# Optimization experiments

Measured on AMD Instinct MI355X. Metric: run time of the kernel, lower is better.

Reference implementation:

```python
import jax, jax.numpy as jnp
import numpy as np

S, B, D, H, E, HID = 512, 16, 768, 12, 8, 3072
HD = D // H
EPS = 1e-5


def _ln(x, w, b):
    m = jnp.mean(x, axis=-1, keepdims=True)
    v = jnp.var(x, axis=-1, keepdims=True)
    return (x - m) * jax.lax.rsqrt(v + EPS) * w + b


def setup_inputs() -> dict:
    key = jax.random.key(0)
    ks = jax.random.split(key, 9)
    n = lambda k, *sh: jax.random.normal(k, sh, dtype=jnp.float32) * 0.02
    return dict(
        x=jax.random.normal(ks[0], (S, B, D), dtype=jnp.float32),
        ln1_w=jnp.ones((D,), jnp.float32), ln1_b=jnp.zeros((D,), jnp.float32),
        wq=n(ks[1], D, D), bq=jnp.zeros((D,), jnp.float32),
        wk=n(ks[2], D, D), bk=jnp.zeros((D,), jnp.float32),
        wv=n(ks[3], D, D), bv=jnp.zeros((D,), jnp.float32),
        wo=n(ks[4], D, D), bo=jnp.zeros((D,), jnp.float32),
        ln2_w=jnp.ones((D,), jnp.float32), ln2_b=jnp.zeros((D,), jnp.float32),
        wg=n(ks[5], D, E), bg=jnp.zeros((E,), jnp.float32),
        w1=n(ks[6], E, D, HID), b1=jnp.zeros((E, HID), jnp.float32),
        w2=n(ks[7], E, HID, D), b2=jnp.zeros((E, D), jnp.float32),
    )


def _block(x, ln1_w, ln1_b, wq, bq, wk, bk, wv, bv, wo, bo,
           ln2_w, ln2_b, wg, bg, w1, b1, w2, b2):
    # --- attention: source uses query = norm1(x), key = value = x ---
    q_in = _ln(x, ln1_w, ln1_b)
    q = (q_in @ wq + bq).reshape(S, B, H, HD)
    k = (x @ wk + bk).reshape(S, B, H, HD)
    v = (x @ wv + bv).reshape(S, B, H, HD)
    scores = jnp.einsum('sbhd,tbhd->bhst', q, k) * (1.0 / HD ** 0.5)
    p = jax.nn.softmax(scores, axis=-1)
    attn = jnp.einsum('bhst,tbhd->sbhd', p, v).reshape(S, B, D)
    x = x + attn @ wo + bo
    # --- top-1 MoE MLP on norm2(x) ---
    t = _ln(x, ln2_w, ln2_b).reshape(S * B, D)   # [T, D] routed tokens
    logits = t @ wg + bg                          # [T, E]
    probs = jax.nn.softmax(logits, axis=-1)
    idx = jnp.argmax(logits, axis=-1)             # top-1 expert per token
    gate = jnp.take_along_axis(probs, idx[:, None], axis=-1)   # [T, 1]
    comb = jax.nn.one_hot(idx, E, dtype=t.dtype) * gate        # [T, E]

    def expert(w1e, b1e, w2e, b2e):
        return jax.nn.gelu(t @ w1e + b1e, approximate=False) @ w2e + b2e

    y = jax.vmap(expert)(w1, b1, w2, b2)          # [E, T, D]
    moe = jnp.einsum('te,etd->td', comb, y).reshape(S, B, D)
    return x + moe


def reference(x, ln1_w, ln1_b, wq, bq, wk, bk, wv, bv, wo, bo,
              ln2_w, ln2_b, wg, bg, w1, b1, w2, b2):
    return _block(x, ln1_w, ln1_b, wq, bq, wk, bk, wv, bv, wo, bo,
                  ln2_w, ln2_b, wg, bg, w1, b1, w2, b2)
```

## Files before the change

kernel.cpp:

```cpp
#include <hip/hip_runtime.h>
#include <math.h>

#define SS 512
#define BB 16
#define DD 768
#define HH 12
#define HDIM 64
#define EE 8
#define HID 3072
#define TT 8192
#define EPSV 1e-5f
#define KVSTR 1536
#define ASTR 72
#define NBANK 64

typedef __attribute__((ext_vector_type(8))) short s16x8;
typedef __attribute__((ext_vector_type(4))) short s16x4;
typedef __attribute__((ext_vector_type(4))) float f32x4;

__device__ inline short f2bf(float f) {
  unsigned u = __builtin_bit_cast(unsigned, f);
  unsigned r = (u + 0x7fffu + ((u >> 16) & 1u)) >> 16;
  return (short)r;
}

__device__ inline float gelu_f(float x) {
  float y = 0.7978845608028654f * (x + 0.044715f * x * x * x);
  float e = __expf(2.f * y);
  float t = 1.f - 2.f / (e + 1.f);
  return 0.5f * x * (1.f + t);
}

__device__ inline void gl2lds16(const void* g, void* l) {
  __builtin_amdgcn_global_load_lds(
      (const __attribute__((address_space(1))) unsigned int*)g,
      (__attribute__((address_space(3))) unsigned int*)l, 16, 0, 0);
}

__global__ __launch_bounds__(256) void transpose4_bf16(const float* __restrict__ w0,
    const float* __restrict__ w1p, const float* __restrict__ w2p,
    const float* __restrict__ w3p, short* __restrict__ dst) {
  const int z = blockIdx.z;
  const float* W = (z == 0) ? w0 : (z == 1) ? w1p : (z == 2) ? w2p : w3p;
  short* Wt = dst + (size_t)z * DD * DD;
  int k0 = blockIdx.x * 64, n0 = blockIdx.y * 64;
  __shared__ float t[64][65];
  for (int i = threadIdx.x; i < 1024; i += 256) {
    int r = i >> 4, c4 = (i & 15) << 2;
    const float4 v = *(const float4*)(W + (size_t)(k0 + r) * DD + n0 + c4);
    t[r][c4] = v.x; t[r][c4 + 1] = v.y; t[r][c4 + 2] = v.z; t[r][c4 + 3] = v.w;
  }
  __syncthreads();
  for (int i = threadIdx.x; i < 1024; i += 256) {
    int r = i >> 4, c4 = (i & 15) << 2;
    s16x4 sv;
    sv.x = f2bf(t[c4][r]);     sv.y = f2bf(t[c4 + 1][r]);
    sv.z = f2bf(t[c4 + 2][r]); sv.w = f2bf(t[c4 + 3][r]);
    *(s16x4*)(Wt + (size_t)(n0 + r) * DD + k0 + c4) = sv;
  }
}

__global__ __launch_bounds__(256) void transpose_bf16(const float* __restrict__ W,
    short* __restrict__ Wt, int K, int N) {
  const float* Wz = W + (size_t)blockIdx.z * K * N;
  short* Wtz = Wt + (size_t)blockIdx.z * K * N;
  int k0 = blockIdx.x * 64, n0 = blockIdx.y * 64;
  __shared__ float t[64][65];
  for (int i = threadIdx.x; i < 1024; i += 256) {
    int r = i >> 4, c4 = (i & 15) << 2;
    const float4 v = *(const float4*)(Wz + (size_t)(k0 + r) * N + n0 + c4);
    t[r][c4] = v.x; t[r][c4 + 1] = v.y; t[r][c4 + 2] = v.z; t[r][c4 + 3] = v.w;
  }
  __syncthreads();
  for (int i = threadIdx.x; i < 1024; i += 256) {
    int r = i >> 4, c4 = (i & 15) << 2;
    s16x4 sv;
    sv.x = f2bf(t[c4][r]);     sv.y = f2bf(t[c4 + 1][r]);
    sv.z = f2bf(t[c4 + 2][r]); sv.w = f2bf(t[c4 + 3][r]);
    *(s16x4*)(Wtz + (size_t)(n0 + r) * K + k0 + c4) = sv;
  }
}

__global__ __launch_bounds__(256) void gate_transpose(const float* __restrict__ wg,
    float* __restrict__ wgT) {
  for (int i = threadIdx.x + blockIdx.x * 256; i < EE * DD; i += 256 * 8) {
    int e = i / DD, d = i - e * DD;
    wgT[i] = wg[d * EE + e];
  }
}

__global__ __launch_bounds__(256) void fused_cvt_ln1(const float* __restrict__ x,
    const float* __restrict__ w, const float* __restrict__ b,
    short* __restrict__ xbf, short* __restrict__ ln1bf) {
  const int tok = blockIdx.x * 4 + (threadIdx.x >> 6);
  const int lane = threadIdx.x & 63;
  const float* row = x + (size_t)tok * DD;
  const float4 v0 = *(const float4*)(row + lane * 4);
  const float4 v1 = *(const float4*)(row + 256 + lane * 4);
  const float4 v2 = *(const float4*)(row + 512 + lane * 4);
  float s = v0.x + v0.y + v0.z + v0.w + v1.x + v1.y + v1.z + v1.w
          + v2.x + v2.y + v2.z + v2.w;
  float ss = v0.x * v0.x + v0.y * v0.y + v0.z * v0.z + v0.w * v0.w
           + v1.x * v1.x + v1.y * v1.y + v1.z * v1.z + v1.w * v1.w
           + v2.x * v2.x + v2.y * v2.y + v2.z * v2.z + v2.w * v2.w;
#pragma unroll
  for (int o = 1; o < 64; o <<= 1) { s += __shfl_xor(s, o); ss += __shfl_xor(ss, o); }
  const float mean = s * (1.f / DD);
  const float inv = rsqrtf(ss * (1.f / DD) - mean * mean + EPSV);
  short* xrow = xbf + (size_t)tok * DD;
  short* lrow = ln1bf + (size_t)tok * DD;
#define LN1_CHUNK(v, off) { \
  const float4 wv = *(const float4*)(w + (off) + lane * 4); \
  const float4 bv = *(const float4*)(b + (off) + lane * 4); \
  s16x4 xa, la; \
  xa.x = f2bf(v.x); xa.y = f2bf(v.y); xa.z = f2bf(v.z); xa.w = f2bf(v.w); \
  la.x = f2bf((v.x - mean) * inv * wv.x + bv.x); \
  la.y = f2bf((v.y - mean) * inv * wv.y + bv.y); \
  la.z = f2bf((v.z - mean) * inv * wv.z + bv.z); \
  la.w = f2bf((v.w - mean) * inv * wv.w + bv.w); \
  *(s16x4*)(xrow + (off) + lane * 4) = xa; \
  *(s16x4*)(lrow + (off) + lane * 4) = la; }
  LN1_CHUNK(v0, 0)
  LN1_CHUNK(v1, 256)
  LN1_CHUNK(v2, 512)
#undef LN1_CHUNK
}

__global__ __launch_bounds__(256) void fused_ln2_route(const float* __restrict__ x1,
    const float* __restrict__ w, const float* __restrict__ b,
    const float* __restrict__ wgT, const float* __restrict__ bg,
    short* __restrict__ tlnbf, int* __restrict__ idx, float* __restrict__ gate,
    int* __restrict__ cnt2) {
  const int tok = blockIdx.x * 4 + (threadIdx.x >> 6);
  const int lane = threadIdx.x & 63;
  const float* row = x1 + (size_t)tok * DD;
  const float4 v0 = *(const float4*)(row + lane * 4);
  const float4 v1 = *(const float4*)(row + 256 + lane * 4);
  const float4 v2 = *(const float4*)(row + 512 + lane * 4);
  float s = v0.x + v0.y + v0.z + v0.w + v1.x + v1.y + v1.z + v1.w
          + v2.x + v2.y + v2.z + v2.w;
  float ss = v0.x * v0.x + v0.y * v0.y + v0.z * v0.z + v0.w * v0.w
           + v1.x * v1.x + v1.y * v1.y + v1.z * v1.z + v1.w * v1.w
           + v2.x * v2.x + v2.y * v2.y + v2.z * v2.z + v2.w * v2.w;
#pragma unroll
  for (int o = 1; o < 64; o <<= 1) { s += __shfl_xor(s, o); ss += __shfl_xor(ss, o); }
  const float mean = s * (1.f / DD);
  const float inv = rsqrtf(ss * (1.f / DD) - mean * mean + EPSV);
  short* srow = tlnbf + (size_t)tok * DD;
  float acc[EE];
#pragma unroll
  for (int e = 0; e < EE; ++e) acc[e] = 0.f;
#define LN2_CHUNK(v, off) { \
  const float4 wv = *(const float4*)(w + (off) + lane * 4); \
  const float4 bv = *(const float4*)(b + (off) + lane * 4); \
  float4 n; \
  n.x = (v.x - mean) * inv * wv.x + bv.x; \
  n.y = (v.y - mean) * inv * wv.y + bv.y; \
  n.z = (v.z - mean) * inv * wv.z + bv.z; \
  n.w = (v.w - mean) * inv * wv.w + bv.w; \
  s16x4 sv; sv.x = f2bf(n.x); sv.y = f2bf(n.y); sv.z = f2bf(n.z); sv.w = f2bf(n.w); \
  *(s16x4*)(srow + (off) + lane * 4) = sv; \
  const int i0 = (off) + lane * 4; \
  _Pragma("unroll") \
  for (int e = 0; e < EE; ++e) { \
    const float4 g = *(const float4*)(wgT + (size_t)e * DD + i0); \
    acc[e] += n.x * g.x + n.y * g.y + n.z * g.z + n.w * g.w; } }
  LN2_CHUNK(v0, 0)
  LN2_CHUNK(v1, 256)
  LN2_CHUNK(v2, 512)
#undef LN2_CHUNK
#pragma unroll
  for (int o = 1; o < 64; o <<= 1)
#pragma unroll
    for (int e = 0; e < EE; ++e) acc[e] += __shfl_xor(acc[e], o);
  if (lane == 0) {
#pragma unroll
    for (int e = 0; e < EE; ++e) acc[e] += bg[e];
    int best = 0; float bm = acc[0];
#pragma unroll
    for (int e = 1; e < EE; ++e) if (acc[e] > bm) { bm = acc[e]; best = e; }
    float sum = 0.f;
#pragma unroll
    for (int e = 0; e < EE; ++e) sum += __expf(acc[e] - bm);
    idx[tok] = best;
    gate[tok] = 1.0f / sum;
    atomicAdd(&cnt2[(blockIdx.x & (NBANK - 1)) * 16 + best], 1);
  }
}

__global__ void prefix2_kernel(const int* __restrict__ cnt2, int* __restrict__ cnt,
                               int* __restrict__ off, int* __restrict__ tb,
                               int* __restrict__ bankbase) {
  const int lane = threadIdx.x;
  int c[EE], excl[EE], tot[EE];
#pragma unroll
  for (int e = 0; e < EE; ++e) c[e] = cnt2[lane * 16 + e];
#pragma unroll
  for (int e = 0; e < EE; ++e) {
    int x = c[e];
#pragma unroll
    for (int o = 1; o < 64; o <<= 1) {
      int y = __shfl_up(x, o);
      if (lane >= o) x += y;
    }
    excl[e] = x - c[e];
    tot[e] = __shfl(x, 63);
  }
  int oo = 0;
  int offl[EE];
#pragma unroll
  for (int e = 0; e < EE; ++e) { offl[e] = oo; oo += tot[e]; }
#pragma unroll
  for (int e = 0; e < EE; ++e)
    bankbase[lane * EE + e] = offl[e] + excl[e];
  if (lane == 0) {
    int o = 0, t = 0;
    for (int e = 0; e < EE; ++e) {
      off[e] = o; tb[e] = t; cnt[e] = tot[e];
      o += tot[e]; t += (tot[e] + 127) >> 7;
    }
    off[EE] = o; tb[EE] = t;
  }
}

__global__ __launch_bounds__(256) void scatter_kernel(const int* __restrict__ idx,
    const int* __restrict__ bankbase, int* __restrict__ cur2, int* __restrict__ perm) {
  int t = blockIdx.x * 256 + threadIdx.x;
  if (t < TT) {
    int e = idx[t];
    int bank = (t >> 2) & (NBANK - 1);
    int p = atomicAdd(&cur2[bank * 16 + e], 1);
    perm[bankbase[bank * EE + e] + p] = t;
  }
}

template<int MODE, int OUTBF, int COLS>
__global__ __launch_bounds__(256) void mgemm(const short* __restrict__ A,
    const short* __restrict__ Wt, const float* __restrict__ bias,
    const float* __restrict__ bias2, const float* __restrict__ res,
    void* __restrict__ C, int N, int K) {
  const int bx = blockIdx.x;
  const int lid = bx >> 3;
  const int colt = lid >> 3, rband = lid & 7;
  const int bm = (((bx & 7) << 3) + rband) * 128;
  const int bn = colt * COLS;
  constexpr int NJ = COLS / 32;
  __shared__ short As[128 * 32];
  __shared__ short Bs[COLS * 32];
  const int tid = threadIdx.x;
  const int wave = tid >> 6, lane = tid & 63;
  const int wr = (wave >> 1) * 64, wc = (wave & 1) * (COLS / 2);
  const int l16 = lane & 15, quad = lane >> 4;
  const int kq = (((lane & 3) ^ ((lane >> 3) & 3)) << 3);
  const int sw = ((l16 >> 1) & 3);
  const short* Ab = A + (size_t)(bm + (wave << 5) + (lane >> 2)) * K + kq;
  const short* Bb = Wt + (size_t)(bn + wave * (COLS / 4) + (lane >> 2)) * K + kq;
  short* lA = &As[(wave << 5) * 32];
  short* lB = &Bs[wave * (COLS / 4) * 32];
  f32x4 acc[4][NJ] = {};
  for (int k0 = 0; k0 < K; k0 += 32) {
    gl2lds16(Ab + k0, lA);
    gl2lds16(Ab + (size_t)16 * K + k0, lA + 512);
    gl2lds16(Bb + k0, lB);
    if (COLS == 128) gl2lds16(Bb + (size_t)16 * K + k0, lB + 512);
    __syncthreads();
    s16x8 af[4], bfr[NJ];
#pragma unroll
    for (int i = 0; i < 4; ++i)
      af[i] = *(s16x8*)(&As[(wr + i * 16 + l16) * 32 + ((quad ^ sw) << 3)]);
#pragma unroll
    for (int j = 0; j < NJ; ++j)
      bfr[j] = *(s16x8*)(&Bs[(wc + j * 16 + l16) * 32 + ((quad ^ sw) << 3)]);
#pragma unroll
    for (int i = 0; i < 4; ++i)
#pragma unroll
      for (int j = 0; j < NJ; ++j)
        acc[i][j] = __builtin_amdgcn_mfma_f32_16x16x32_bf16(af[i], bfr[j], acc[i][j], 0, 0, 0);
    __syncthreads();
  }
#pragma unroll
  for (int i = 0; i < 4; ++i) {
#pragma unroll
    for (int r = 0; r < 4; ++r) {
      int row = bm + wr + i * 16 + quad * 4 + r;
#pragma unroll
      for (int j = 0; j < NJ; ++j) {
        int col = bn + wc + j * 16 + l16;
        float bv = (MODE == 2) ? (col >= DD ? bias2[col - DD] : bias[col]) : bias[col];
        float val = acc[i][j][r] + bv;
        if (MODE == 1) val += res[(size_t)row * N + col];
        if (OUTBF) ((short*)C)[(size_t)row * N + col] = f2bf(val);
        else       ((float*)C)[(size_t)row * N + col] = val;
      }
    }
  }
}

__global__ __launch_bounds__(512) void qkv_mgemm(const short* __restrict__ ln1bf,
    const short* __restrict__ xbf, const short* __restrict__ wqT,
    const short* __restrict__ kvT, const float* __restrict__ bq,
    const float* __restrict__ bk, const float* __restrict__ bv,
    short* __restrict__ qbf, short* __restrict__ kvbf) {
  const int bx = blockIdx.x;
  const int lid = bx >> 3;
  const int colt = lid >> 3, rband = lid & 7;
  const int bm = (((bx & 7) << 3) + rband) * 128;
  const bool isQ = (colt < 6);
  const int bn = isQ ? colt * 128 : (colt - 6) * 128;
  const short* A  = isQ ? ln1bf : xbf;
  const short* Bt = isQ ? wqT : kvT;
  const float* bias = isQ ? bq : (bn < DD ? bk : bv);
  const int bofs = (!isQ && bn >= DD) ? DD : 0;
  short* out = isQ ? qbf : kvbf;
  const int OS = isQ ? DD : KVSTR;
  const int K = DD;
  __shared__ short As[128 * 64];
  __shared__ short Bs[128 * 64];
  const int tid = threadIdx.x;
  const int wave = tid >> 6, lane = tid & 63;
  const int wr = (wave >> 2) * 64;
  const int wc = (wave & 3) * 32;
  const int l16 = lane & 15, quad = lane >> 4;
  const int rg = lane >> 3;
  const int kq8 = (((lane & 7) ^ rg) << 3);
  const int swz = l16 & 7;
  const short* Ab = A + (size_t)(bm + (wave << 4) + rg) * K + kq8;
  const short* Bb = Bt + (size_t)(bn + (wave << 4) + rg) * K + kq8;
  short* lA = &As[(wave << 4) * 64];
  short* lB = &Bs[(wave << 4) * 64];
  f32x4 acc[4][2] = {};
  for (int k0 = 0; k0 < K; k0 += 64) {
    gl2lds16(Ab + k0, lA);
    gl2lds16(Ab + (size_t)8 * K + k0, lA + 512);
    gl2lds16(Bb + k0, lB);
    gl2lds16(Bb + (size_t)8 * K + k0, lB + 512);
    __syncthreads();
#pragma unroll
    for (int h = 0; h < 2; ++h) {
      s16x8 af[4], bfr[2];
#pragma unroll
      for (int i = 0; i < 4; ++i)
        af[i] = *(s16x8*)(&As[(wr + i * 16 + l16) * 64 + (((quad + 4 * h) ^ swz) << 3)]);
#pragma unroll
      for (int j = 0; j < 2; ++j)
        bfr[j] = *(s16x8*)(&Bs[(wc + j * 16 + l16) * 64 + (((quad + 4 * h) ^ swz) << 3)]);
#pragma unroll
      for (int i = 0; i < 4; ++i)
#pragma unroll
        for (int j = 0; j < 2; ++j)
          acc[i][j] = __builtin_amdgcn_mfma_f32_16x16x32_bf16(af[i], bfr[j], acc[i][j], 0, 0, 0);
    }
    __syncthreads();
  }
#pragma unroll
  for (int i = 0; i < 4; ++i) {
#pragma unroll
    for (int r = 0; r < 4; ++r) {
      int row = bm + wr + i * 16 + quad * 4 + r;
#pragma unroll
      for (int j = 0; j < 2; ++j) {
        int col = bn + wc + j * 16 + l16;
        float val = acc[i][j][r] + bias[col - bofs];
        out[(size_t)row * OS + col] = f2bf(val);
      }
    }
  }
}

__global__ __launch_bounds__(256) void attn_mfma(const short* __restrict__ q,
    const short* __restrict__ k, const short* __restrict__ v, short* __restrict__ o) {
  const int qt = blockIdx.x, bidx = blockIdx.y, hidx = blockIdx.z;
  const int tid = threadIdx.x;
  const int wave = tid >> 6, lane = tid & 63;
  const int l16 = lane & 15, quad = lane >> 4;
  const int s0 = qt * 64;
  __shared__ short Qs[64 * ASTR];
  __shared__ short Ks[64 * ASTR];
  __shared__ short Vs[64 * ASTR];
  __shared__ short Ps[64 * ASTR];
  for (int i = tid; i < 512; i += 256) {
    int r = i >> 3, c8 = i & 7;
    *(s16x8*)(&Qs[r * ASTR + c8 * 8]) =
        *(const s16x8*)(q + ((size_t)(s0 + r) * BB + bidx) * DD + hidx * HDIM + c8 * 8);
  }
  __syncthreads();
  s16x8 af0 = *(s16x8*)(&Qs[(wave * 16 + l16) * ASTR + quad * 8]);
  s16x8 af1 = *(s16x8*)(&Qs[(wave * 16 + l16) * ASTR + 32 + quad * 8]);
  f32x4 oacc[4] = {};
  float mr[4], lr[4];
#pragma unroll
  for (int r = 0; r < 4; ++r) { mr[r] = -1e30f; lr[r] = 0.f; }

  for (int t0 = 0; t0 < SS; t0 += 64) {
    __syncthreads();
    for (int i = tid; i < 512; i += 256) {
      int r = i >> 3, c8 = i & 7;
      *(s16x8*)(&Ks[r * ASTR + c8 * 8]) =
          *(const s16x8*)(k + ((size_t)(t0 + r) * BB + bidx) * KVSTR + hidx * HDIM + c8 * 8);
    }
    for (int i = tid; i < 1024; i += 256) {
      int r = i >> 4, c4 = i & 15;
      s16x4 vv = *(const s16x4*)(v + ((size_t)(t0 + r) * BB + bidx) * KVSTR + hidx * HDIM + c4 * 4);
      Vs[(c4 * 4 + 0) * ASTR + r] = vv.x;
      Vs[(c4 * 4 + 1) * ASTR + r] = vv.y;
      Vs[(c4 * 4 + 2) * ASTR + r] = vv.z;
      Vs[(c4 * 4 + 3) * ASTR + r] = vv.w;
    }
    __syncthreads();
    f32x4 sc[4];
    const f32x4 zero = {};
#pragma unroll
    for (int j = 0; j < 4; ++j) {
      s16x8 kf0 = *(s16x8*)(&Ks[(j * 16 + l16) * ASTR + quad * 8]);
      s16x8 kf1 = *(s16x8*)(&Ks[(j * 16 + l16) * ASTR + 32 + quad * 8]);
      sc[j] = __builtin_amdgcn_mfma_f32_16x16x32_bf16(af0, kf0, zero, 0, 0, 0);
      sc[j] = __builtin_amdgcn_mfma_f32_16x16x32_bf16(af1, kf1, sc[j], 0, 0, 0);
#pragma unroll
      for (int r = 0; r < 4; ++r) sc[j][r] *= 0.125f;
    }
    float tm[4], alpha[4], rs[4];
#pragma unroll
    for (int r = 0; r < 4; ++r) {
      tm[r] = mr[r];
#pragma unroll
      for (int j = 0; j < 4; ++j) tm[r] = fmaxf(tm[r], sc[j][r]);
    }
#pragma unroll
    for (int mask = 1; mask < 16; mask <<= 1)
#pragma unroll
      for (int r = 0; r < 4; ++r) tm[r] = fmaxf(tm[r], __shfl_xor(tm[r], mask));
#pragma unroll
    for (int r = 0; r < 4; ++r) { alpha[r] = __expf(mr[r] - tm[r]); mr[r] = tm[r]; rs[r] = 0.f; }
#pragma unroll
    for (int j = 0; j < 4; ++j)
#pragma unroll
      for (int r = 0; r < 4; ++r) {
        float p = __expf(sc[j][r] - tm[r]);
        sc[j][r] = p; rs[r] += p;
      }
#pragma unroll
    for (int mask = 1; mask < 16; mask <<= 1)
#pragma unroll
      for (int r = 0; r < 4; ++r) rs[r] += __shfl_xor(rs[r], mask);
#pragma unroll
    for (int r = 0; r < 4; ++r) lr[r] = lr[r] * alpha[r] + rs[r];
#pragma unroll
    for (int j = 0; j < 4; ++j)
#pragma unroll
      for (int r = 0; r < 4; ++r)
        Ps[(wave * 16 + quad * 4 + r) * ASTR + j * 16 + l16] = f2bf(sc[j][r]);
#pragma unroll
    for (int jd = 0; jd < 4; ++jd)
#pragma unroll
      for (int r = 0; r < 4; ++r) oacc[jd][r] *= alpha[r];
    __syncthreads();
    s16x8 pf0 = *(s16x8*)(&Ps[(wave * 16 + l16) * ASTR + quad * 8]);
    s16x8 pf1 = *(s16x8*)(&Ps[(wave * 16 + l16) * ASTR + 32 + quad * 8]);
#pragma unroll
    for (int jd = 0; jd < 4; ++jd) {
      s16x8 vf0 = *(s16x8*)(&Vs[(jd * 16 + l16) * ASTR + quad * 8]);
      s16x8 vf1 = *(s16x8*)(&Vs[(jd * 16 + l16) * ASTR + 32 + quad * 8]);
      oacc[jd] = __builtin_amdgcn_mfma_f32_16x16x32_bf16(pf0, vf0, oacc[jd], 0, 0, 0);
      oacc[jd] = __builtin_amdgcn_mfma_f32_16x16x32_bf16(pf1, vf1, oacc[jd], 0, 0, 0);
    }
  }
#pragma unroll
  for (int r = 0; r < 4; ++r) {
    int row = s0 + wave * 16 + quad * 4 + r;
    float invl = 1.f / lr[r];
#pragma unroll
    for (int jd = 0; jd < 4; ++jd) {
      int d = jd * 16 + l16;
      o[((size_t)row * BB + bidx) * DD + hidx * HDIM + d] = f2bf(oacc[jd][r] * invl);
    }
  }
}

__global__ __launch_bounds__(512) void egemm1(const short* __restrict__ tlnbf,
    const short* __restrict__ w1t, const float* __restrict__ b1,
    const int* __restrict__ off, const int* __restrict__ tb, const int* __restrict__ cnt,
    const int* __restrict__ perm, short* __restrict__ hbuf) {
  const int bx = blockIdx.x;
  const int lid = bx >> 3;
  const int rband = lid % 9, colt = lid / 9;
  const int row = (bx & 7) * 9 + rband;
  if (row >= tb[EE]) return;
  int e = 0;
  while (e < EE - 1 && tb[e + 1] <= row) ++e;
  const int lt = row - tb[e];
  const int cnte = cnt[e];
  const int slot0 = off[e] + lt * 128;
  const int slast = off[e] + cnte - 1;
  const int bn = colt * 128;
  const int tid = threadIdx.x;
  const int wave = tid >> 6, lane = tid & 63;
  const int wr = (wave >> 2) * 64;
  const int wc = (wave & 3) * 32;
  const int l16 = lane & 15, quad = lane >> 4;
  const int rg = lane >> 3;
  const int kq8 = (((lane & 7) ^ rg) << 3);
  const int swz = l16 & 7;
  __shared__ short As[128 * 64];
  __shared__ short Bs[128 * 64];
  f32x4 acc[4][2] = {};
  const int sA0 = slot0 + (wave << 4) + rg;
  const int tokA = perm[sA0 <= slast ? sA0 : slast];
  const int tokB = perm[(sA0 + 8) <= slast ? (sA0 + 8) : slast];
  const short* AbA = tlnbf + (size_t)tokA * DD + kq8;
  const short* AbB = tlnbf + (size_t)tokB * DD + kq8;
  const short* Bb = w1t + (size_t)e * DD * HID
                  + (size_t)(bn + (wave << 4) + rg) * DD + kq8;
  short* lA = &As[(wave << 4) * 64];
  short* lB = &Bs[(wave << 4) * 64];
  for (int k0 = 0; k0 < DD; k0 += 64) {
    gl2lds16(AbA + k0, lA);
    gl2lds16(AbB + k0, lA + 512);
    gl2lds16(Bb + k0, lB);
    gl2lds16(Bb + (size_t)8 * DD + k0, lB + 512);
    __syncthreads();
#pragma unroll
    for (int h = 0; h < 2; ++h) {
      s16x8 af[4], bfr[2];
#pragma unroll
      for (int i = 0; i < 4; ++i)
        af[i] = *(s16x8*)(&As[(wr + i * 16 + l16) * 64 + (((quad + 4 * h) ^ swz) << 3)]);
#pragma unroll
      for (int j = 0; j < 2; ++j)
        bfr[j] = *(s16x8*)(&Bs[(wc + j * 16 + l16) * 64 + (((quad + 4 * h) ^ swz) << 3)]);
#pragma unroll
      for (int i = 0; i < 4; ++i)
#pragma unroll
        for (int j = 0; j < 2; ++j)
          acc[i][j] = __builtin_amdgcn_mfma_f32_16x16x32_bf16(af[i], bfr[j], acc[i][j], 0, 0, 0);
    }
    __syncthreads();
  }
#pragma unroll
  for (int i = 0; i < 4; ++i) {
#pragma unroll
    for (int r = 0; r < 4; ++r) {
      int rl = wr + i * 16 + quad * 4 + r;
      if (lt * 128 + rl >= cnte) continue;
#pragma unroll
      for (int j = 0; j < 2; ++j) {
        int col = bn + wc + j * 16 + l16;
        float xv = acc[i][j][r] + b1[e * HID + col];
        hbuf[(size_t)(slot0 + rl) * HID + col] = f2bf(gelu_f(xv));
      }
    }
  }
}

__global__ __launch_bounds__(256) void egemm2(const short* __restrict__ hbuf,
    const short* __restrict__ w2t, const float* __restrict__ b2,
    const int* __restrict__ perm, const int* __restrict__ off,
    const int* __restrict__ tb, const int* __restrict__ cnt,
    const float* __restrict__ gate, const float* __restrict__ x1,
    float* __restrict__ out) {
  const int bx = blockIdx.x;
  const int lid = bx >> 3;
  const int colt = lid % 12, rband = lid / 12;
  const int row = (bx & 7) * 9 + rband;
  if (row >= tb[EE]) return;
  int e = 0;
  while (e < EE - 1 && tb[e + 1] <= row) ++e;
  const int lt = row - tb[e];
  const int cnte = cnt[e];
  const int slot0 = off[e] + lt * 128;
  const int bn = colt * 64;
  const int tid = threadIdx.x;
  const int wave = tid >> 6, lane = tid & 63;
  const int wr = (wave >> 1) * 64, wc = (wave & 1) * 32;
  const int l16 = lane & 15, quad = lane >> 4;
  const int rg = lane >> 3;
  const int kq8 = (((lane & 7) ^ rg) << 3);
  const int swz = l16 & 7;
  __shared__ short As[128 * 64];
  __shared__ short Bs[64 * 64];
  __shared__ int stok[128];
  if (tid < 128) stok[tid] = (lt * 128 + tid < cnte) ? perm[slot0 + tid] : -1;
  f32x4 acc[4][2] = {};
  const short* Ab = hbuf + (size_t)(slot0 + (wave << 5) + rg) * HID + kq8;
  const short* Bb = w2t + (size_t)e * HID * DD
                  + (size_t)(bn + wave * 16 + rg) * HID + kq8;
  short* lA = &As[(wave << 5) * 64];
  short* lB = &Bs[wave * 16 * 64];
  for (int k0 = 0; k0 < HID; k0 += 64) {
    gl2lds16(Ab + k0, lA);
    gl2lds16(Ab + (size_t)8 * HID + k0, lA + 512);
    gl2lds16(Ab + (size_t)16 * HID + k0, lA + 1024);
    gl2lds16(Ab + (size_t)24 * HID + k0, lA + 1536);
    gl2lds16(Bb + k0, lB);
    gl2lds16(Bb + (size_t)8 * HID + k0, lB + 512);
    __syncthreads();
#pragma unroll
    for (int h = 0; h < 2; ++h) {
      s16x8 af[4], bfr[2];
#pragma unroll
      for (int i = 0; i < 4; ++i)
        af[i] = *(s16x8*)(&As[(wr + i * 16 + l16) * 64 + (((quad + 4 * h) ^ swz) << 3)]);
#pragma unroll
      for (int j = 0; j < 2; ++j)
        bfr[j] = *(s16x8*)(&Bs[(wc + j * 16 + l16) * 64 + (((quad + 4 * h) ^ swz) << 3)]);
#pragma unroll
      for (int i = 0; i < 4; ++i)
#pragma unroll
        for (int j = 0; j < 2; ++j)
          acc[i][j] = __builtin_amdgcn_mfma_f32_16x16x32_bf16(af[i], bfr[j], acc[i][j], 0, 0, 0);
    }
    __syncthreads();
  }
#pragma unroll
  for (int i = 0; i < 4; ++i) {
#pragma unroll
    for (int r = 0; r < 4; ++r) {
      int rl = wr + i * 16 + quad * 4 + r;
      if (lt * 128 + rl >= cnte) continue;
      int tok = stok[rl];
      float g = gate[tok];
#pragma unroll
      for (int j = 0; j < 2; ++j) {
        int col = bn + wc + j * 16 + l16;
        float val = acc[i][j][r] + b2[e * DD + col];
        out[(size_t)tok * DD + col] = x1[(size_t)tok * DD + col] + g * val;
      }
    }
  }
}

extern "C" void kernel_launch(void* const* d_in, const int* in_sizes, int n_in,
                              void* d_out, int out_size, void* d_ws, size_t ws_size,
                              hipStream_t stream) {
  const float* x     = (const float*)d_in[0];
  const float* ln1_w = (const float*)d_in[1];
  const float* ln1_b = (const float*)d_in[2];
  const float* wq    = (const float*)d_in[3];
  const float* bq    = (const float*)d_in[4];
  const float* wk    = (const float*)d_in[5];
  const float* bk    = (const float*)d_in[6];
  const float* wv    = (const float*)d_in[7];
  const float* bv    = (const float*)d_in[8];
  const float* wo    = (const float*)d_in[9];
  const float* bo    = (const float*)d_in[10];
  const float* ln2_w = (const float*)d_in[11];
  const float* ln2_b = (const float*)d_in[12];
  const float* wg    = (const float*)d_in[13];
  const float* bg    = (const float*)d_in[14];
  const float* w1    = (const float*)d_in[15];
  const float* b1    = (const float*)d_in[16];
  const float* w2    = (const float*)d_in[17];
  const float* b2    = (const float*)d_in[18];
  float* out = (float*)d_out;
  float* ws = (float*)d_ws;

  const size_t TD = (size_t)TT * DD;
  float* x1    = ws;
  short* tlnbf = (short*)(ws + TD);
  short* sbase = (short*)(ws + 2 * TD);
  short* xbf   = sbase;
  short* ln1bf = sbase + TD + 128 * DD;
  short* attbf = ln1bf;
  short* qbf   = ln1bf + TD;
  short* kvbf  = qbf + TD;
  short* hbuf  = kvbf + (size_t)TT * KVSTR;
  short* wqT   = hbuf + (size_t)(TT + 128) * HID;
  short* kvT   = wqT + (size_t)DD * DD;
  short* woT   = kvT + (size_t)KVSTR * DD;
  short* w1T   = woT + (size_t)DD * DD;
  short* w2T   = w1T + (size_t)EE * DD * HID;
  int*   meta  = (int*)(w2T + (size_t)EE * HID * DD);
  int*   idx   = meta;
  float* gate  = (float*)(meta + TT);
  int*   perm  = meta + 2 * TT;
  int*   cnt2  = meta + 3 * TT;
  int*   cur2  = cnt2 + NBANK * 16;
  int*   bankbase = cur2 + NBANK * 16;
  int*   cnt   = bankbase + NBANK * EE;
  int*   off   = cnt + 8;
  int*   tb    = off + 9;
  float* wgT   = (float*)(tb + 9);

  hipMemsetAsync(cnt2, 0, 2 * NBANK * 16 * sizeof(int), stream);

  transpose4_bf16<<<dim3(12, 12, 4), 256, 0, stream>>>(wq, wk, wv, wo, wqT);
  transpose_bf16<<<dim3(12, 48, 8), 256, 0, stream>>>(w1, w1T, DD, HID);
  transpose_bf16<<<dim3(48, 12, 8), 256, 0, stream>>>(w2, w2T, HID, DD);
  gate_transpose<<<8, 256, 0, stream>>>(wg, wgT);

  fused_cvt_ln1<<<TT / 4, 256, 0, stream>>>(x, ln1_w, ln1_b, xbf, ln1bf);

  qkv_mgemm<<<8 * 8 * 18, 512, 0, stream>>>(ln1bf, xbf, wqT, kvT, bq, bk, bv, qbf, kvbf);

  attn_mfma<<<dim3(SS / 64, BB, HH), 256, 0, stream>>>(qbf, kvbf, kvbf + DD, attbf);

  mgemm<1, 0, 64><<<64 * 12, 256, 0, stream>>>(attbf, woT, bo, nullptr, x, x1, DD, DD);

  fused_ln2_route<<<TT / 4, 256, 0, stream>>>(x1, ln2_w, ln2_b, wgT, bg,
                                              tlnbf, idx, gate, cnt2);
  prefix2_kernel<<<1, 64, 0, stream>>>(cnt2, cnt, off, tb, bankbase);
  scatter_kernel<<<TT / 256, 256, 0, stream>>>(idx, bankbase, cur2, perm);

  egemm1<<<8 * 9 * 24, 512, 0, stream>>>(tlnbf, w1T, b1, off, tb, cnt, perm, hbuf);
  egemm2<<<8 * 9 * 12, 256, 0, stream>>>(hbuf, w2T, b2, perm, off, tb, cnt, gate, x1, out);
}
```

Measured before the change: 539.9 us.

## Split-K the second expert GEMM with atomic accumulation into pre-seeded output

The second expert GEMM is split into two halves along the hidden dimension, doubling the grid so more blocks run concurrently on the GPU. Each half atomically adds its gated partial result into the output. To make this work, the output projection GEMM now also writes the residual x1 into the output buffer, so the experts only need to accumulate onto it. The cost is float atomics on every output element, an extra full write of the residual, and a summation order that is no longer deterministic.

```diff
diff --git a/kernel.cpp b/kernel.cpp
--- a/kernel.cpp
+++ b/kernel.cpp
@@ -13,6 +13,7 @@
 #define KVSTR 1536
 #define ASTR 72
 #define NBANK 64
+#define E2GRID (8 * 9 * 12)
 
 typedef __attribute__((ext_vector_type(8))) short s16x8;
 typedef __attribute__((ext_vector_type(4))) short s16x4;
@@ -234,11 +235,11 @@
   }
 }
 
-template<int MODE, int OUTBF, int COLS>
+template<int MODE, int OUTBF, int COLS, int DUP>
 __global__ __launch_bounds__(256) void mgemm(const short* __restrict__ A,
     const short* __restrict__ Wt, const float* __restrict__ bias,
     const float* __restrict__ bias2, const float* __restrict__ res,
-    void* __restrict__ C, int N, int K) {
+    void* __restrict__ C, float* __restrict__ dup, int N, int K) {
   const int bx = blockIdx.x;
   const int lid = bx >> 3;
   const int colt = lid >> 3, rband = lid & 7;
@@ -290,7 +291,10 @@
         float val = acc[i][j][r] + bv;
         if (MODE == 1) val += res[(size_t)row * N + col];
         if (OUTBF) ((short*)C)[(size_t)row * N + col] = f2bf(val);
-        else       ((float*)C)[(size_t)row * N + col] = val;
+        else {
+          ((float*)C)[(size_t)row * N + col] = val;
+          if (DUP) dup[(size_t)row * N + col] = val;
+        }
       }
     }
   }
@@ -555,9 +559,10 @@
     const short* __restrict__ w2t, const float* __restrict__ b2,
     const int* __restrict__ perm, const int* __restrict__ off,
     const int* __restrict__ tb, const int* __restrict__ cnt,
-    const float* __restrict__ gate, const float* __restrict__ x1,
-    float* __restrict__ out) {
-  const int bx = blockIdx.x;
+    const float* __restrict__ gate, float* __restrict__ out) {
+  const int bxr = blockIdx.x;
+  const int ks = (bxr >= E2GRID) ? 1 : 0;
+  const int bx = bxr - ks * E2GRID;
   const int lid = bx >> 3;
   const int colt = lid % 12, rband = lid / 12;
   const int row = (bx & 7) * 9 + rband;
@@ -568,6 +573,7 @@
   const int cnte = cnt[e];
   const int slot0 = off[e] + lt * 128;
   const int bn = colt * 64;
+  const int kbase = ks * (HID / 2);
   const int tid = threadIdx.x;
   const int wave = tid >> 6, lane = tid & 63;
   const int wr = (wave >> 1) * 64, wc = (wave & 1) * 32;
@@ -580,12 +586,12 @@
   __shared__ int stok[128];
   if (tid < 128) stok[tid] = (lt * 128 + tid < cnte) ? perm[slot0 + tid] : -1;
   f32x4 acc[4][2] = {};
-  const short* Ab = hbuf + (size_t)(slot0 + (wave << 5) + rg) * HID + kq8;
+  const short* Ab = hbuf + (size_t)(slot0 + (wave << 5) + rg) * HID + kbase + kq8;
   const short* Bb = w2t + (size_t)e * HID * DD
-                  + (size_t)(bn + wave * 16 + rg) * HID + kq8;
+                  + (size_t)(bn + wave * 16 + rg) * HID + kbase + kq8;
   short* lA = &As[(wave << 5) * 64];
   short* lB = &Bs[wave * 16 * 64];
-  for (int k0 = 0; k0 < HID; k0 += 64) {
+  for (int k0 = 0; k0 < HID / 2; k0 += 64) {
     gl2lds16(Ab + k0, lA);
     gl2lds16(Ab + (size_t)8 * HID + k0, lA + 512);
     gl2lds16(Ab + (size_t)16 * HID + k0, lA + 1024);
@@ -621,8 +627,8 @@
 #pragma unroll
       for (int j = 0; j < 2; ++j) {
         int col = bn + wc + j * 16 + l16;
-        float val = acc[i][j][r] + b2[e * DD + col];
-        out[(size_t)tok * DD + col] = x1[(size_t)tok * DD + col] + g * val;
+        float val = acc[i][j][r] + (ks ? 0.f : b2[e * DD + col]);
+        atomicAdd(&out[(size_t)tok * DD + col], g * val);
       }
     }
   }
@@ -693,7 +699,8 @@
 
   attn_mfma<<<dim3(SS / 64, BB, HH), 256, 0, stream>>>(qbf, kvbf, kvbf + DD, attbf);
 
-  mgemm<1, 0, 64><<<64 * 12, 256, 0, stream>>>(attbf, woT, bo, nullptr, x, x1, DD, DD);
+  mgemm<1, 0, 64, 1><<<64 * 12, 256, 0, stream>>>(attbf, woT, bo, nullptr, x,
+                                                  x1, out, DD, DD);
 
   fused_ln2_route<<<TT / 4, 256, 0, stream>>>(x1, ln2_w, ln2_b, wgT, bg,
                                               tlnbf, idx, gate, cnt2);
@@ -701,5 +708,5 @@
   scatter_kernel<<<TT / 256, 256, 0, stream>>>(idx, bankbase, cur2, perm);
 
   egemm1<<<8 * 9 * 24, 512, 0, stream>>>(tlnbf, w1T, b1, off, tb, cnt, perm, hbuf);
-  egemm2<<<8 * 9 * 12, 256, 0, stream>>>(hbuf, w2T, b2, perm, off, tb, cnt, gate, x1, out);
-}
+  egemm2<<<E2GRID * 2, 256, 0, stream>>>(hbuf, w2T, b2, perm, off, tb, cnt, gate, out);
+}
```

Measured after the change: 570.9 us. 5.7% more time.
